# Performance work log

Hardware: AMD Instinct MI355X
Metric: run time of the kernel (lower is better)

The kernel has to match this reference:

```python
import jax, jax.numpy as jnp
from jax import lax
import numpy as np

B, N, NPOINTS, DOWN_NUM, K = 4, 4096, 4096, 1024, 16
EPS = 1e-5


def setup_inputs() -> dict:
    key = jax.random.key(0)
    ks = jax.random.split(key, 8)
    w = lambda k, s: jax.random.normal(k, s, jnp.float32) * 0.05
    return {
        "x": jax.random.normal(ks[0], (B, 3, N), jnp.float32),
        "w_in": w(ks[1], (8, 3)), "b_in": jnp.zeros((8,), jnp.float32),
        "w1": w(ks[2], (32, 16)), "g1w": jnp.ones((32,), jnp.float32), "g1b": jnp.zeros((32,), jnp.float32),
        "w2": w(ks[3], (64, 64)), "g2w": jnp.ones((64,), jnp.float32), "g2b": jnp.zeros((64,), jnp.float32),
        "w3": w(ks[4], (64, 128)), "g3w": jnp.ones((64,), jnp.float32), "g3b": jnp.zeros((64,), jnp.float32),
        "w4": w(ks[5], (128, 128)), "g4w": jnp.ones((128,), jnp.float32), "g4b": jnp.zeros((128,), jnp.float32),
    }


def _knn_idx(coor_k, coor_q, k):
    # coor_*: (B,3,N) -> idx (B,Nq,k) of k nearest points in coor_k for each query
    q = coor_q.transpose(0, 2, 1)  # (B,Nq,3)
    r = coor_k.transpose(0, 2, 1)  # (B,Nk,3)
    d = (jnp.sum(q * q, -1)[:, :, None] + jnp.sum(r * r, -1)[:, None, :]
         - 2.0 * jnp.einsum('bqc,bkc->bqk', q, r))
    _, idx = lax.top_k(-d, k)  # smallest distances
    return idx


def _graph_feature(coor_q, x_q, coor_k, x_k, k):
    # gather k-NN neighbor features and concat (neighbor - center, center)
    idx = _knn_idx(coor_k, coor_q, k)           # (B,Nq,k)
    xk = x_k.transpose(0, 2, 1)                  # (B,Nk,C)
    b, nq, _ = idx.shape
    c = xk.shape[-1]
    feat = jnp.take_along_axis(xk, idx.reshape(b, nq * k)[..., None], axis=1)
    feat = feat.reshape(b, nq, k, c).transpose(0, 3, 1, 2)  # (B,C,Nq,k)
    xq = x_q[:, :, :, None]                      # (B,C,Nq,1)
    return jnp.concatenate([feat - xq, jnp.broadcast_to(xq, feat.shape)], axis=1)


def _fps_idx(xyz, m):
    # furthest point sampling, xyz (B,N,3) -> idx (B,m); starts at point 0
    b, n, _ = xyz.shape
    def body(carry, _):
        dists, farthest = carry
        centroid = jnp.take_along_axis(xyz, farthest[:, None, None], axis=1)  # (B,1,3)
        d = jnp.sum((xyz - centroid) ** 2, axis=-1)
        dists = jnp.minimum(dists, d)
        return (dists, jnp.argmax(dists, axis=-1)), farthest
    init = (jnp.full((b, n), 1e10, xyz.dtype), jnp.zeros((b,), jnp.int32))
    _, idx = lax.scan(body, init, None, length=m)
    return idx.T  # (B,m)


def _fps_downsample(coor, f, m):
    idx = _fps_idx(coor.transpose(0, 2, 1), m)        # (B,m)
    combined = jnp.concatenate([coor, f], axis=1)      # (B,3+C,N)
    new = jnp.take_along_axis(combined, idx[:, None, :], axis=2)
    return new[:, :3], new[:, 3:]


def _group_norm(x, w, b, groups=4):
    bsz, c = x.shape[0], x.shape[1]
    xr = x.reshape(bsz, groups, -1)
    m = xr.mean(-1, keepdims=True)
    v = xr.var(-1, keepdims=True)
    xn = ((xr - m) * lax.rsqrt(v + EPS)).reshape(x.shape)
    shp = (1, c) + (1,) * (x.ndim - 2)
    return xn * w.reshape(shp) + b.reshape(shp)


def _block(f, w, gw, gb):
    # 1x1 conv (no bias) -> GroupNorm(4) -> LeakyReLU(0.2) -> max over neighbors
    h = jnp.einsum('oc,bcnk->bonk', w, f)
    h = jax.nn.leaky_relu(_group_norm(h, gw, gb), negative_slope=0.2)
    return h.max(axis=-1)


def reference(x, w_in, b_in, w1, g1w, g1b, w2, g2w, g2b, w3, g3w, g3b, w4, g4w, g4b):
    coor = x
    f = jnp.einsum('oc,bcn->bon', w_in, x) + b_in[None, :, None]
    inpc_f = f
    f = _graph_feature(coor, f, coor, f, K)
    f = _block(f, w1, g1w, g1b)                      # (B,32,N)
    coor_q, f_q = _fps_downsample(coor, f, NPOINTS // 2)
    f = _graph_feature(coor_q, f_q, coor, f, K)
    f = _block(f, w2, g2w, g2b)                      # (B,64,N/2)
    xyz1, point1 = coor_q, f
    coor = coor_q
    f = _graph_feature(coor, f, coor, f, K)
    f = _block(f, w3, g3w, g3b)                      # (B,64,N/2)
    coor_q, f_q = _fps_downsample(coor, f, DOWN_NUM)
    f = _graph_feature(coor_q, f_q, coor, f, K)
    f = _block(f, w4, g4w, g4b)                      # (B,128,DOWN_NUM)
    coor = coor_q
    return (coor, f, xyz1, point1, inpc_f)
```

## Files before the change

### kernel.cpp

```cpp
#include <hip/hip_runtime.h>
#include <float.h>
#include <math.h>

static constexpr int BATCH = 4;
static constexpr int NPT0  = 4096;

static constexpr size_t OFF_F0T  = 0;
static constexpr size_t OFF_F1T  = 524288;
static constexpr size_t OFF_F2T  = 3670016;
static constexpr size_t OFF_F3T  = 5767168;
static constexpr size_t OFF_CQ1  = 8912896;
static constexpr size_t OFF_CQ2  = 9011200;
static constexpr size_t OFF_H    = 9060352;
static constexpr size_t OFF_IDX1 = 42614784;
static constexpr size_t OFF_IDX2 = 43663360;
static constexpr size_t OFF_IDX3 = 44187648;
static constexpr size_t OFF_IDX4 = 44711936;
static constexpr size_t OFF_FPS1 = 44974080;
static constexpr size_t OFF_FPS2 = 45006848;
static constexpr size_t OFF_WD1  = 45023232;
static constexpr size_t OFF_WD2  = 45024256;
static constexpr size_t OFF_WD3  = 45032448;
static constexpr size_t OFF_WD4  = 45048832;
static constexpr size_t OFF_STAT = 45081600;
static constexpr size_t OFF_PART  = 45099008;
static constexpr size_t OFF_PART2 = OFF_PART;
static constexpr size_t OFF_PART3 = OFF_PART + 4194304;
static constexpr size_t OFF_PART4 = OFF_PART + 6291456;
static constexpr size_t OFF_CAND0 = 53487616;
static constexpr size_t OFF_CAND1 = 53749760;

static constexpr size_t OUT_COOR = 0;
static constexpr size_t OUT_F    = 12288;
static constexpr size_t OUT_XYZ1 = 536576;
static constexpr size_t OUT_PT1  = 561152;
static constexpr size_t OUT_INPC = 1085440;

template<int CTRL>
__device__ __forceinline__ unsigned long long dpp_max64(unsigned long long k) {
  unsigned lo = (unsigned)k, hi = (unsigned)(k >> 32);
  unsigned olo = (unsigned)__builtin_amdgcn_update_dpp((int)lo, (int)lo, CTRL, 0xF, 0xF, false);
  unsigned ohi = (unsigned)__builtin_amdgcn_update_dpp((int)hi, (int)hi, CTRL, 0xF, 0xF, false);
  unsigned long long o = ((unsigned long long)ohi << 32) | olo;
  return o > k ? o : k;
}

__device__ __forceinline__ void prep_dev(
    int vb, const float* __restrict__ w1, const float* __restrict__ w2,
    const float* __restrict__ w3, const float* __restrict__ w4,
    float* __restrict__ wd1, float* __restrict__ wd2,
    float* __restrict__ wd3, float* __restrict__ wd4,
    double* __restrict__ stats)
{
  int t = vb * 256 + threadIdx.x;
  if (t < 128) stats[t] = 0.0;
  if (t < 32 * 8)   { int o = t / 8,  c = t % 8;  wd1[t] = w1[o*16  + 8   + c] - w1[o*16  + c]; }
  if (t < 64 * 32)  { int o = t / 32, c = t % 32; wd2[t] = w2[o*64  + 32  + c] - w2[o*64  + c]; }
  if (t < 64 * 64)  { int o = t / 64, c = t % 64; wd3[t] = w3[o*128 + 64  + c] - w3[o*128 + c]; }
  if (t < 128 * 64) { int o = t / 64, c = t % 64; wd4[t] = w4[o*128 + 64  + c] - w4[o*128 + c]; }
}

__device__ __forceinline__ void linear_dev(
    int vb, const float* __restrict__ x, const float* __restrict__ w_in,
    const float* __restrict__ b_in, float* __restrict__ f0t,
    float* __restrict__ out_inpc)
{
  int t = vb * 256 + threadIdx.x;
  int n = t & (NPT0 - 1);
  int b = t >> 12;
  float x0 = x[(size_t)b*3*NPT0 + n];
  float x1 = x[(size_t)b*3*NPT0 + NPT0 + n];
  float x2 = x[(size_t)b*3*NPT0 + 2*NPT0 + n];
#pragma unroll
  for (int o = 0; o < 8; ++o) {
    float v = __fmul_rn(w_in[o*3], x0);
    v = fmaf(w_in[o*3+1], x1, v);
    v = fmaf(w_in[o*3+2], x2, v);
    v = __fadd_rn(v, b_in[o]);
    f0t[(size_t)t * 8 + o] = v;
    out_inpc[((size_t)b*8 + o)*NPT0 + n] = v;
  }
}

template<int CS>
__device__ __forceinline__ void knnp_pack_dev(
    int vb, const float* __restrict__ cq, const float4* __restrict__ candPack,
    unsigned long long* __restrict__ part, int Nq, int Nk)
{
  const int slices = Nk / CS;
  int s  = vb % slices;
  int r  = vb / slices;
  int qb = r % (Nq >> 8);
  int b  = r / (Nq >> 8);
  int t  = threadIdx.x;
  int q  = qb*256 + t;
  const float* cqb = cq + (size_t)b*3*Nq;
  float qx = cqb[q], qy = cqb[Nq + q], qz = cqb[2*Nq + q];
  float sqq = __fadd_rn(__fadd_rn(__fmul_rn(qx,qx), __fmul_rn(qy,qy)), __fmul_rn(qz,qz));

  const float4* cp = candPack + (size_t)b*Nk + s*CS;
  int jbase = s*CS;

  unsigned long long bd[16];
#pragma unroll
  for (int sl = 0; sl < 16; ++sl) bd[sl] = ~0ull;
  unsigned long long wk = ~0ull; int ws = 0;

#pragma unroll 4
  for (int jj = 0; jj < CS; ++jj) {
    float4 c = cp[jj];
    float dot = __fmul_rn(c.x, qx);
    dot = fmaf(c.y, qy, dot);
    dot = fmaf(c.z, qz, dot);
    float d = __fsub_rn(__fadd_rn(sqq, c.w), __fmul_rn(2.0f, dot));
    unsigned u = __float_as_uint(d);
    u ^= (0x80000000u | (unsigned)((int)u >> 31));
    unsigned long long key = ((unsigned long long)u << 32) | (unsigned)(jbase + jj);
    if (key < wk) {
      unsigned long long nw = 0; int nws = 0;
#pragma unroll
      for (int sl = 0; sl < 16; ++sl) {
        bool rep = (sl == ws);
        unsigned long long v = rep ? key : bd[sl];
        bd[sl] = v;
        bool g = v > nw;
        nw = g ? v : nw; nws = g ? sl : nws;
      }
      wk = nw; ws = nws;
    }
  }
  unsigned long long* op = part + (((size_t)b*Nq + q)*(size_t)slices + s)*16;
#pragma unroll
  for (int sl = 0; sl < 16; ++sl) op[sl] = bd[sl];
}

__device__ __forceinline__ void knnp_lds_dev(
    int vb, const float* __restrict__ cq, const float* __restrict__ ck,
    unsigned long long* __restrict__ part, int Nq, int Nk, int slices, void* smem)
{
  const int CS = 512;
  int s  = vb % slices;
  int r  = vb / slices;
  int qb = r % (Nq >> 8);
  int b  = r / (Nq >> 8);
  float4* cand = (float4*)smem;
  int t = threadIdx.x;
  const float* ckb = ck + (size_t)b*3*Nk;
  for (int jj = t; jj < CS; jj += 256) {
    int j = s*CS + jj;
    float xx = ckb[j], yy = ckb[Nk + j], zz = ckb[2*Nk + j];
    float sq = __fadd_rn(__fadd_rn(__fmul_rn(xx,xx), __fmul_rn(yy,yy)), __fmul_rn(zz,zz));
    cand[jj] = make_float4(xx, yy, zz, sq);
  }
  __syncthreads();
  int q = qb*256 + t;
  const float* cqb = cq + (size_t)b*3*Nq;
  float qx = cqb[q], qy = cqb[Nq + q], qz = cqb[2*Nq + q];
  float sqq = __fadd_rn(__fadd_rn(__fmul_rn(qx,qx), __fmul_rn(qy,qy)), __fmul_rn(qz,qz));

  unsigned long long bd[16];
#pragma unroll
  for (int sl = 0; sl < 16; ++sl) bd[sl] = ~0ull;
  unsigned long long wk = ~0ull; int ws = 0;

  for (int jj = 0; jj < CS; ++jj) {
    float4 c = cand[jj];
    float dot = __fmul_rn(c.x, qx);
    dot = fmaf(c.y, qy, dot);
    dot = fmaf(c.z, qz, dot);
    float d = __fsub_rn(__fadd_rn(sqq, c.w), __fmul_rn(2.0f, dot));
    unsigned u = __float_as_uint(d);
    u ^= (0x80000000u | (unsigned)((int)u >> 31));
    unsigned long long key = ((unsigned long long)u << 32) | (unsigned)(s*CS + jj);
    if (key < wk) {
      unsigned long long nw = 0; int nws = 0;
#pragma unroll
      for (int sl = 0; sl < 16; ++sl) {
        bool rep = (sl == ws);
        unsigned long long v = rep ? key : bd[sl];
        bd[sl] = v;
        bool g = v > nw;
        nw = g ? v : nw; nws = g ? sl : nws;
      }
      wk = nw; ws = nws;
    }
  }
  unsigned long long* op = part + (((size_t)b*Nq + q)*(size_t)slices + s)*16;
#pragma unroll
  for (int sl = 0; sl < 16; ++sl) op[sl] = bd[sl];
}

__device__ __forceinline__ void merge_dev(
    int vb, const unsigned long long* __restrict__ part, int* __restrict__ idx,
    int slices)
{
  int t = vb * 256 + threadIdx.x;
  const unsigned long long* ip = part + (size_t)t * slices * 16;
  unsigned long long bd[16];
#pragma unroll
  for (int sl = 0; sl < 16; ++sl) bd[sl] = ~0ull;
  unsigned long long wk = ~0ull; int ws = 0;
  int n = slices * 16;
  for (int i = 0; i < n; ++i) {
    unsigned long long key = ip[i];
    if (key < wk) {
      unsigned long long nw = 0; int nws = 0;
#pragma unroll
      for (int sl = 0; sl < 16; ++sl) {
        bool rep = (sl == ws);
        unsigned long long v = rep ? key : bd[sl];
        bd[sl] = v;
        bool g = v > nw;
        nw = g ? v : nw; nws = g ? sl : nws;
      }
      wk = nw; ws = nws;
    }
  }
  int* op = idx + (size_t)t * 16;
#pragma unroll
  for (int sl = 0; sl < 16; ++sl) op[sl] = (int)(bd[sl] & 0xFFFFFFFFull);
}

template<int NN, int PPT>
__device__ __forceinline__ void fps_dev(
    int b, const float* __restrict__ coor, int m, int* __restrict__ fidx_all,
    float* __restrict__ ca_all, float* __restrict__ co_all, void* smem)
{
  float* sx = (float*)smem;
  float* sy = sx + NN;
  float* sz = sy + NN;
  unsigned long long* part = (unsigned long long*)(sz + NN);
  int t = threadIdx.x, lane = t & 63, wv = t >> 6;
  const float* cb = coor + (size_t)b*3*NN;
  float px[PPT], py[PPT], pz[PPT], pd[PPT];
#pragma unroll
  for (int i = 0; i < PPT; ++i) {
    int j = i*256 + t;
    px[i] = cb[j]; py[i] = cb[NN + j]; pz[i] = cb[2*NN + j];
    pd[i] = 1e10f;
    sx[j] = px[i]; sy[j] = py[i]; sz[j] = pz[i];
  }
  __syncthreads();
  float cx = sx[0], cy = sy[0], cz = sz[0];
  int* fidx = fidx_all + b*m;
  float* ca = ca_all + (size_t)b*3*m;
  float* co = co_all + (size_t)b*3*m;
  int cur = 0, par = 0;
  for (int it = 0; it < m; ++it) {
    if (t == 0) {
      fidx[it] = cur;
      ca[it] = cx; ca[m + it] = cy; ca[2*m + it] = cz;
      co[it] = cx; co[m + it] = cy; co[2*m + it] = cz;
    }
    float bv = -1.0f; int bslot = 0;
#pragma unroll
    for (int i = 0; i < PPT; ++i) {
      float dx = __fsub_rn(px[i], cx);
      float dy = __fsub_rn(py[i], cy);
      float dz = __fsub_rn(pz[i], cz);
      float d = __fadd_rn(__fadd_rn(__fmul_rn(dx,dx), __fmul_rn(dy,dy)), __fmul_rn(dz,dz));
      float nd = fminf(pd[i], d);
      pd[i] = nd;
      bool g = nd > bv;
      bv = g ? nd : bv;
      bslot = g ? i : bslot;
    }
    unsigned bij = ~(unsigned)((bslot << 8) | t);
    unsigned long long k = ((unsigned long long)__float_as_uint(bv) << 32) | bij;
    k = dpp_max64<0x111>(k);
    k = dpp_max64<0x112>(k);
    k = dpp_max64<0x114>(k);
    k = dpp_max64<0x118>(k);
    k = dpp_max64<0x142>(k);
    k = dpp_max64<0x143>(k);
    unsigned wlo = (unsigned)__builtin_amdgcn_readlane((int)(unsigned)k, 63);
    unsigned whi = (unsigned)__builtin_amdgcn_readlane((int)(unsigned)(k >> 32), 63);
    if (lane == 0) part[par*4 + wv] = ((unsigned long long)whi << 32) | wlo;
    __syncthreads();
    unsigned long long k0 = part[par*4 + 0], k1 = part[par*4 + 1];
    unsigned long long k2 = part[par*4 + 2], k3 = part[par*4 + 3];
    k0 = k1 > k0 ? k1 : k0;
    k2 = k3 > k2 ? k3 : k2;
    k0 = k2 > k0 ? k2 : k0;
    cur = (int)(~(unsigned)(k0 & 0xFFFFFFFFull));
    cx = sx[cur]; cy = sy[cur]; cz = sz[cur];
    par ^= 1;
  }
}

template<int C, int COUT, int OC>
__device__ __forceinline__ void passA_dev(
    int vb, const float* __restrict__ xq, const float* __restrict__ xk,
    const int* __restrict__ idx, const float* __restrict__ w,
    const float* __restrict__ wdl, float* __restrict__ h,
    double* __restrict__ stats, int Nq, int Nk,
    const int* __restrict__ qmap, int NqSrc, void* smem)
{
  constexpr int NCH = COUT / OC;
  constexpr int GS  = COUT / 4;
  float* sxq   = (float*)smem;
  float* sbase = sxq + 16*C;
  int qb = Nq >> 4;
  int b = vb / qb, nb = vb % qb;
  int n0 = nb << 4;
  int t = threadIdx.x;
  for (int i = t; i < 16*C; i += 256) {
    int nn = i / C, cc = i % C;
    int qrow = qmap ? qmap[b*Nq + n0 + nn] : (n0 + nn);
    sxq[nn*C + cc] = xq[((size_t)b*NqSrc + qrow)*C + cc];
  }
  __syncthreads();
  for (int i = t; i < 16*COUT; i += 256) {
    int nn = i / COUT, o = i % COUT;
    float acc = 0.f;
#pragma unroll 4
    for (int c = 0; c < C; ++c) acc = fmaf(wdl[o*C + c], sxq[nn*C + c], acc);
    sbase[nn*(COUT+1) + o] = acc;
  }
  __syncthreads();
  int lane = t & 63;
  int n_loc = t >> 4, kk = t & 15;
  int kidx = idx[((size_t)b*Nq + n0 + n_loc)*16 + kk];
  const float* xr = xk + ((size_t)b*Nk + kidx)*C;
  float* hrow = h + (((size_t)b*Nq + n0 + n_loc)*16 + kk)*(size_t)COUT;
#pragma unroll 1
  for (int oc = 0; oc < NCH; ++oc) {
    int o0 = oc * OC;
    float acc[OC];
#pragma unroll
    for (int oi = 0; oi < OC; ++oi) acc[oi] = sbase[n_loc*(COUT+1) + o0 + oi];
#pragma unroll 1
    for (int c4 = 0; c4 < C/4; ++c4) {
      float4 v = *(const float4*)(xr + c4*4);
#pragma unroll
      for (int oi = 0; oi < OC; ++oi) {
        const float* wr = w + (size_t)(o0 + oi)*(2*C) + c4*4;
        acc[oi] = fmaf(wr[0], v.x, acc[oi]);
        acc[oi] = fmaf(wr[1], v.y, acc[oi]);
        acc[oi] = fmaf(wr[2], v.z, acc[oi]);
        acc[oi] = fmaf(wr[3], v.w, acc[oi]);
      }
    }
#pragma unroll
    for (int oi = 0; oi < OC; ++oi) hrow[o0 + oi] = acc[oi];
    double s = 0.0, s2 = 0.0;
#pragma unroll
    for (int oi = 0; oi < OC; ++oi) { double dv = (double)acc[oi]; s += dv; s2 += dv*dv; }
#pragma unroll
    for (int mm = 1; mm < 64; mm <<= 1) {
      s  += __shfl_xor(s,  mm, 64);
      s2 += __shfl_xor(s2, mm, 64);
    }
    if (lane == 0) {
      int g = o0 / GS;
      atomicAdd(&stats[((size_t)b*4 + g)*2],     s);
      atomicAdd(&stats[((size_t)b*4 + g)*2 + 1], s2);
    }
  }
}

template<int C, int COUT, int OC>
__global__ __launch_bounds__(256) void k_passA(
    const float* __restrict__ xq, const float* __restrict__ xk,
    const int* __restrict__ idx, const float* __restrict__ w,
    const float* __restrict__ wdl, float* __restrict__ h,
    double* __restrict__ stats, int Nq, int Nk,
    const int* __restrict__ qmap, int NqSrc)
{
  extern __shared__ char smem[];
  passA_dev<C,COUT,OC>(blockIdx.x, xq, xk, idx, w, wdl, h, stats, Nq, Nk,
                       qmap, NqSrc, smem);
}

__device__ __forceinline__ void passB_dev(
    int vb, const float* __restrict__ h, const double* __restrict__ stats,
    const float* __restrict__ gw, const float* __restrict__ gb,
    float* __restrict__ ft, float* __restrict__ ocn, int Nq, int COUT)
{
  int t = vb * 256 + threadIdx.x;
  int o = t % COUT;
  int r = t / COUT;
  int n = r % Nq;
  int b = r / Nq;
  int GS = COUT / 4, g = o / GS;
  double cnt = (double)GS * (double)Nq * 16.0;
  double su = stats[((size_t)b*4 + g)*2];
  double s2 = stats[((size_t)b*4 + g)*2 + 1];
  double mean = su / cnt;
  double var = s2 / cnt - mean * mean;
  float vf = (float)var; if (vf < 0.f) vf = 0.f;
  float inv = 1.0f / sqrtf(vf + 1e-5f);
  float A = gw[o] * inv;
  float Bb = gb[o] - (float)mean * A;
  const float* hp = h + (((size_t)b*Nq + n)*16)*(size_t)COUT + o;
  float m = -FLT_MAX;
#pragma unroll
  for (int k = 0; k < 16; ++k) {
    float v = hp[(size_t)k*COUT];
    float y = fmaf(v, A, Bb);
    y = (y >= 0.f) ? y : 0.2f*y;
    m = fmaxf(m, y);
  }
  if (ft)  ft[((size_t)b*Nq + n)*COUT + o] = m;
  if (ocn) ocn[((size_t)b*COUT + o)*Nq + n] = m;
}

__global__ __launch_bounds__(256) void k_passB(
    const float* __restrict__ h, const double* __restrict__ stats,
    const float* __restrict__ gw, const float* __restrict__ gb,
    float* __restrict__ ft, float* __restrict__ ocn, int Nq, int COUT)
{
  passB_dev(blockIdx.x, h, stats, gw, gb, ft, ocn, Nq, COUT);
}

__global__ __launch_bounds__(256) void k_pre(
    const float* __restrict__ x, const float* __restrict__ w_in,
    const float* __restrict__ b_in, float* __restrict__ f0t,
    float* __restrict__ outInpc,
    const float* __restrict__ w1, const float* __restrict__ w2,
    const float* __restrict__ w3, const float* __restrict__ w4,
    float* __restrict__ wd1, float* __restrict__ wd2,
    float* __restrict__ wd3, float* __restrict__ wd4,
    double* __restrict__ stats, float4* __restrict__ cand0)
{
  int vb = blockIdx.x;
  if (vb < 64) {
    int g = vb*256 + threadIdx.x;
    int b = g >> 12, n = g & 4095;
    const float* xb = x + (size_t)b*3*4096;
    float xx = xb[n], yy = xb[4096 + n], zz = xb[2*4096 + n];
    float sq = __fadd_rn(__fadd_rn(__fmul_rn(xx,xx), __fmul_rn(yy,yy)), __fmul_rn(zz,zz));
    cand0[g] = make_float4(xx, yy, zz, sq);
  }
  else if (vb < 96) prep_dev(vb - 64, w1, w2, w3, w4, wd1, wd2, wd3, wd4, stats);
  else              linear_dev(vb - 96, x, w_in, b_in, f0t, outInpc);
}

__global__ __launch_bounds__(256, 2) void k_megaA(
    const float* __restrict__ x, int* __restrict__ fps1,
    float* __restrict__ cq1, float* __restrict__ outXyz1,
    const float4* __restrict__ cand0, unsigned long long* __restrict__ part1)
{
  extern __shared__ char smem[];
  int vb = blockIdx.x;
  if (vb < 4) fps_dev<4096,16>(vb, x, 2048, fps1, cq1, outXyz1, smem);
  else        knnp_pack_dev<1024>(vb - 4, x, cand0, part1, 4096, 4096);
}

__global__ __launch_bounds__(256) void k_mergeP(
    const unsigned long long* __restrict__ part1, int* __restrict__ idx1,
    const float* __restrict__ cq1, float4* __restrict__ cand1)
{
  int vb = blockIdx.x;
  if (vb < 64) merge_dev(vb, part1, idx1, 4);
  else {
    int g = (vb - 64)*256 + threadIdx.x;
    int b = g >> 11, n = g & 2047;
    const float* cb = cq1 + (size_t)b*3*2048;
    float xx = cb[n], yy = cb[2048 + n], zz = cb[2*2048 + n];
    float sq = __fadd_rn(__fadd_rn(__fmul_rn(xx,xx), __fmul_rn(yy,yy)), __fmul_rn(zz,zz));
    cand1[g] = make_float4(xx, yy, zz, sq);
  }
}

__global__ __launch_bounds__(256, 2) void k_megaB(
    const float* __restrict__ cq1, const float4* __restrict__ cand0,
    const float4* __restrict__ cand1,
    int* __restrict__ fps2, float* __restrict__ cq2, float* __restrict__ outCoor,
    unsigned long long* __restrict__ part2, unsigned long long* __restrict__ part3,
    const float* __restrict__ f0t, const int* __restrict__ idx1,
    const float* __restrict__ w1, const float* __restrict__ wd1,
    float* __restrict__ h, double* __restrict__ st1)
{
  extern __shared__ char smem[];
  int vb = blockIdx.x;
  if      (vb < 4)          fps_dev<2048,8>(vb, cq1, 1024, fps2, cq2, outCoor, smem);
  else if (vb < 4 + 128)    knnp_pack_dev<1024>(vb - 4,   cq1, cand0, part2, 2048, 4096);
  else if (vb < 4 + 128+64) knnp_pack_dev<1024>(vb - 132, cq1, cand1, part3, 2048, 2048);
  else                      passA_dev<8,32,8>(vb - 196, f0t, f0t, idx1, w1, wd1,
                                              h, st1, 4096, 4096, nullptr, 4096, smem);
}

__global__ __launch_bounds__(256) void k_megaC(
    const float* __restrict__ cq2, const float* __restrict__ cq1,
    unsigned long long* __restrict__ part4,
    const unsigned long long* __restrict__ part2, int* __restrict__ idx2,
    const unsigned long long* __restrict__ part3, int* __restrict__ idx3,
    const float* __restrict__ h, const double* __restrict__ st1,
    const float* __restrict__ g1w, const float* __restrict__ g1b,
    float* __restrict__ f1t)
{
  extern __shared__ char smem[];
  int vb = blockIdx.x;
  if      (vb < 64)  knnp_lds_dev(vb, cq2, cq1, part4, 1024, 2048, 4, smem);
  else if (vb < 96)  merge_dev(vb - 64, part2, idx2, 4);
  else if (vb < 128) merge_dev(vb - 96, part3, idx3, 2);
  else               passB_dev(vb - 128, h, st1, g1w, g1b, f1t, nullptr, 4096, 32);
}

__global__ __launch_bounds__(256) void k_megaD(
    const unsigned long long* __restrict__ part4, int* __restrict__ idx4,
    const float* __restrict__ f1t, const int* __restrict__ idx2,
    const float* __restrict__ w2, const float* __restrict__ wd2,
    float* __restrict__ h, double* __restrict__ st2,
    const int* __restrict__ fps1)
{
  extern __shared__ char smem[];
  int vb = blockIdx.x;
  if (vb < 16) merge_dev(vb, part4, idx4, 4);
  else         passA_dev<32,64,16>(vb - 16, f1t, f1t, idx2, w2, wd2, h, st2,
                                   2048, 4096, fps1, 4096, smem);
}

extern "C" void kernel_launch(void* const* d_in, const int* in_sizes, int n_in,
                              void* d_out, int out_size, void* d_ws, size_t ws_size,
                              hipStream_t stream)
{
  (void)in_sizes; (void)n_in; (void)out_size; (void)ws_size;
  const float* x    = (const float*)d_in[0];
  const float* w_in = (const float*)d_in[1];
  const float* b_in = (const float*)d_in[2];
  const float* w1   = (const float*)d_in[3];
  const float* g1w  = (const float*)d_in[4];
  const float* g1b  = (const float*)d_in[5];
  const float* w2   = (const float*)d_in[6];
  const float* g2w  = (const float*)d_in[7];
  const float* g2b  = (const float*)d_in[8];
  const float* w3   = (const float*)d_in[9];
  const float* g3w  = (const float*)d_in[10];
  const float* g3b  = (const float*)d_in[11];
  const float* w4   = (const float*)d_in[12];
  const float* g4w  = (const float*)d_in[13];
  const float* g4b  = (const float*)d_in[14];
  float* out = (float*)d_out;
  char*  wsb = (char*)d_ws;

  float* f0t  = (float*)(wsb + OFF_F0T);
  float* f1t  = (float*)(wsb + OFF_F1T);
  float* f2t  = (float*)(wsb + OFF_F2T);
  float* f3t  = (float*)(wsb + OFF_F3T);
  float* cq1  = (float*)(wsb + OFF_CQ1);
  float* cq2  = (float*)(wsb + OFF_CQ2);
  float* h    = (float*)(wsb + OFF_H);
  int*   idx1 = (int*)(wsb + OFF_IDX1);
  int*   idx2 = (int*)(wsb + OFF_IDX2);
  int*   idx3 = (int*)(wsb + OFF_IDX3);
  int*   idx4 = (int*)(wsb + OFF_IDX4);
  int*   fps1 = (int*)(wsb + OFF_FPS1);
  int*   fps2 = (int*)(wsb + OFF_FPS2);
  float* wd1  = (float*)(wsb + OFF_WD1);
  float* wd2  = (float*)(wsb + OFF_WD2);
  float* wd3  = (float*)(wsb + OFF_WD3);
  float* wd4  = (float*)(wsb + OFF_WD4);
  double* statAll = (double*)(wsb + OFF_STAT);
  double* st1 = statAll, *st2 = statAll + 32, *st3 = statAll + 64, *st4 = statAll + 96;
  unsigned long long* part1 = (unsigned long long*)(wsb + OFF_PART);
  unsigned long long* part2 = (unsigned long long*)(wsb + OFF_PART2);
  unsigned long long* part3 = (unsigned long long*)(wsb + OFF_PART3);
  unsigned long long* part4 = (unsigned long long*)(wsb + OFF_PART4);
  float4* cand0 = (float4*)(wsb + OFF_CAND0);
  float4* cand1 = (float4*)(wsb + OFF_CAND1);

  float* outCoor = out + OUT_COOR;
  float* outF    = out + OUT_F;
  float* outXyz1 = out + OUT_XYZ1;
  float* outPt1  = out + OUT_PT1;
  float* outInpc = out + OUT_INPC;

  k_pre<<<160, 256, 0, stream>>>(x, w_in, b_in, f0t, outInpc,
      w1, w2, w3, w4, wd1, wd2, wd3, wd4, statAll, cand0);

  k_megaA<<<260, 256, 49216, stream>>>(x, fps1, cq1, outXyz1, cand0, part1);

  k_mergeP<<<96, 256, 0, stream>>>(part1, idx1, cq1, cand1);

  k_megaB<<<1220, 256, 24640, stream>>>(
      cq1, cand0, cand1, fps2, cq2, outCoor, part2, part3, f0t, idx1, w1, wd1, h, st1);

  k_megaC<<<2176, 256, 8192, stream>>>(
      cq2, cq1, part4, part2, idx2, part3, idx3, h, st1, g1w, g1b, f1t);

  k_megaD<<<528, 256, 6208, stream>>>(part4, idx4, f1t, idx2, w2, wd2, h, st2, fps1);

  k_passB<<<2048, 256, 0, stream>>>(h, st2, g2w, g2b, f2t, outPt1, 2048, 64);
  k_passA<64,64,16><<<512, 256, 8256, stream>>>(f2t, f2t, idx3, w3, wd3, h, st3,
                                                2048, 2048, nullptr, 2048);
  k_passB<<<2048, 256, 0, stream>>>(h, st3, g3w, g3b, f3t, nullptr, 2048, 64);
  k_passA<64,128,16><<<256, 256, 12352, stream>>>(f3t, f3t, idx4, w4, wd4, h, st4,
                                                  1024, 2048, fps2, 2048);
  k_passB<<<2048, 256, 0, stream>>>(h, st4, g4w, g4b, nullptr, outF, 1024, 128);
}
```

Baseline: 3.037 ms.

## Widen FPS and KNN mega-kernel blocks to 512 threads

Furthest point sampling now runs with 512 threads per block instead of 256. Each thread holds half as many points, and the cross-wave argmax reduction loops over 8 wave partials. The KNN partial kernels handle 512 queries per block, and two 256-thread passA sub-blocks are packed into one 512-thread block, each with its own shared-memory region. The goal is to shorten the serial FPS iteration chain and reduce the number of blocks launched. The cost is a wider per-iteration reduction, the loss of the 2-blocks-per-CU occupancy hint, and a dependence on any unshown code in the KNN path that may still assume 256 threads.

```diff
diff --git a/kernel.cpp b/kernel.cpp
--- a/kernel.cpp
+++ b/kernel.cpp
@@ -83,17 +83,17 @@
 }
 
 template<int CS>
-__device__ __forceinline__ void knnp_pack_dev(
+__device__ __forceinline__ void knnp_pack_dev512(
     int vb, const float* __restrict__ cq, const float4* __restrict__ candPack,
     unsigned long long* __restrict__ part, int Nq, int Nk)
 {
   const int slices = Nk / CS;
   int s  = vb % slices;
   int r  = vb / slices;
-  int qb = r % (Nq >> 8);
-  int b  = r / (Nq >> 8);
+  int qb = r % (Nq >> 9);
+  int b  = r / (Nq >> 9);
   int t  = threadIdx.x;
-  int q  = qb*256 + t;
+  int q  = qb*512 + t;
   const float* cqb = cq + (size_t)b*3*Nq;
   float qx = cqb[q], qy = cqb[Nq + q], qz = cqb[2*Nq + q];
   float sqq = __fadd_rn(__fadd_rn(__fmul_rn(qx,qx), __fmul_rn(qy,qy)), __fmul_rn(qz,qz));
@@ -221,11 +221,12 @@
   for (int sl = 0; sl < 16; ++sl) op[sl] = (int)(bd[sl] & 0xFFFFFFFFull);
 }
 
-template<int NN, int PPT>
+template<int NN, int PPT, int NTHR>
 __device__ __forceinline__ void fps_dev(
     int b, const float* __restrict__ coor, int m, int* __restrict__ fidx_all,
     float* __restrict__ ca_all, float* __restrict__ co_all, void* smem)
 {
+  constexpr int WAVES = NTHR / 64;
   float* sx = (float*)smem;
   float* sy = sx + NN;
   float* sz = sy + NN;
@@ -235,7 +236,7 @@
   float px[PPT], py[PPT], pz[PPT], pd[PPT];
 #pragma unroll
   for (int i = 0; i < PPT; ++i) {
-    int j = i*256 + t;
+    int j = i*NTHR + t;
     px[i] = cb[j]; py[i] = cb[NN + j]; pz[i] = cb[2*NN + j];
     pd[i] = 1e10f;
     sx[j] = px[i]; sy[j] = py[i]; sz[j] = pz[i];
@@ -265,7 +266,7 @@
       bv = g ? nd : bv;
       bslot = g ? i : bslot;
     }
-    unsigned bij = ~(unsigned)((bslot << 8) | t);
+    unsigned bij = ~(unsigned)(bslot * NTHR + t);
     unsigned long long k = ((unsigned long long)__float_as_uint(bv) << 32) | bij;
     k = dpp_max64<0x111>(k);
     k = dpp_max64<0x112>(k);
@@ -275,13 +276,14 @@
     k = dpp_max64<0x143>(k);
     unsigned wlo = (unsigned)__builtin_amdgcn_readlane((int)(unsigned)k, 63);
     unsigned whi = (unsigned)__builtin_amdgcn_readlane((int)(unsigned)(k >> 32), 63);
-    if (lane == 0) part[par*4 + wv] = ((unsigned long long)whi << 32) | wlo;
+    if (lane == 0) part[par*WAVES + wv] = ((unsigned long long)whi << 32) | wlo;
     __syncthreads();
-    unsigned long long k0 = part[par*4 + 0], k1 = part[par*4 + 1];
-    unsigned long long k2 = part[par*4 + 2], k3 = part[par*4 + 3];
-    k0 = k1 > k0 ? k1 : k0;
-    k2 = k3 > k2 ? k3 : k2;
-    k0 = k2 > k0 ? k2 : k0;
+    unsigned long long k0 = part[par*WAVES + 0];
+#pragma unroll
+    for (int w = 1; w < WAVES; ++w) {
+      unsigned long long kw = part[par*WAVES + w];
+      k0 = kw > k0 ? kw : k0;
+    }
     cur = (int)(~(unsigned)(k0 & 0xFFFFFFFFull));
     cx = sx[cur]; cy = sy[cur]; cz = sz[cur];
     par ^= 1;
@@ -290,7 +292,7 @@
 
 template<int C, int COUT, int OC>
 __device__ __forceinline__ void passA_dev(
-    int vb, const float* __restrict__ xq, const float* __restrict__ xk,
+    int vb, int tid, const float* __restrict__ xq, const float* __restrict__ xk,
     const int* __restrict__ idx, const float* __restrict__ w,
     const float* __restrict__ wdl, float* __restrict__ h,
     double* __restrict__ stats, int Nq, int Nk,
@@ -303,7 +305,7 @@
   int qb = Nq >> 4;
   int b = vb / qb, nb = vb % qb;
   int n0 = nb << 4;
-  int t = threadIdx.x;
+  int t = tid;
   for (int i = t; i < 16*C; i += 256) {
     int nn = i / C, cc = i % C;
     int qrow = qmap ? qmap[b*Nq + n0 + nn] : (n0 + nn);
@@ -368,8 +370,8 @@
     const int* __restrict__ qmap, int NqSrc)
 {
   extern __shared__ char smem[];
-  passA_dev<C,COUT,OC>(blockIdx.x, xq, xk, idx, w, wdl, h, stats, Nq, Nk,
-                       qmap, NqSrc, smem);
+  passA_dev<C,COUT,OC>(blockIdx.x, threadIdx.x, xq, xk, idx, w, wdl, h, stats,
+                       Nq, Nk, qmap, NqSrc, smem);
 }
 
 __device__ __forceinline__ void passB_dev(
@@ -436,15 +438,15 @@
   else              linear_dev(vb - 96, x, w_in, b_in, f0t, outInpc);
 }
 
-__global__ __launch_bounds__(256, 2) void k_megaA(
+__global__ __launch_bounds__(512) void k_megaA(
     const float* __restrict__ x, int* __restrict__ fps1,
     float* __restrict__ cq1, float* __restrict__ outXyz1,
     const float4* __restrict__ cand0, unsigned long long* __restrict__ part1)
 {
   extern __shared__ char smem[];
   int vb = blockIdx.x;
-  if (vb < 4) fps_dev<4096,16>(vb, x, 2048, fps1, cq1, outXyz1, smem);
-  else        knnp_pack_dev<1024>(vb - 4, x, cand0, part1, 4096, 4096);
+  if (vb < 4) fps_dev<4096,8,512>(vb, x, 2048, fps1, cq1, outXyz1, smem);
+  else        knnp_pack_dev512<1024>(vb - 4, x, cand0, part1, 4096, 4096);
 }
 
 __global__ __launch_bounds__(256) void k_mergeP(
@@ -463,7 +465,7 @@
   }
 }
 
-__global__ __launch_bounds__(256, 2) void k_megaB(
+__global__ __launch_bounds__(512) void k_megaB(
     const float* __restrict__ cq1, const float4* __restrict__ cand0,
     const float4* __restrict__ cand1,
     int* __restrict__ fps2, float* __restrict__ cq2, float* __restrict__ outCoor,
@@ -474,11 +476,16 @@
 {
   extern __shared__ char smem[];
   int vb = blockIdx.x;
-  if      (vb < 4)          fps_dev<2048,8>(vb, cq1, 1024, fps2, cq2, outCoor, smem);
-  else if (vb < 4 + 128)    knnp_pack_dev<1024>(vb - 4,   cq1, cand0, part2, 2048, 4096);
-  else if (vb < 4 + 128+64) knnp_pack_dev<1024>(vb - 132, cq1, cand1, part3, 2048, 2048);
-  else                      passA_dev<8,32,8>(vb - 196, f0t, f0t, idx1, w1, wd1,
-                                              h, st1, 4096, 4096, nullptr, 4096, smem);
+  if      (vb < 4)         fps_dev<2048,4,512>(vb, cq1, 1024, fps2, cq2, outCoor, smem);
+  else if (vb < 4 + 64)    knnp_pack_dev512<1024>(vb - 4,  cq1, cand0, part2, 2048, 4096);
+  else if (vb < 4 + 64+32) knnp_pack_dev512<1024>(vb - 68, cq1, cand1, part3, 2048, 2048);
+  else {
+    int sub = threadIdx.x >> 8;
+    int tid = threadIdx.x & 255;
+    int vpa = (vb - 100)*2 + sub;
+    passA_dev<8,32,8>(vpa, tid, f0t, f0t, idx1, w1, wd1,
+                      h, st1, 4096, 4096, nullptr, 4096, smem + sub*2624);
+  }
 }
 
 __global__ __launch_bounds__(256) void k_megaC(
@@ -508,8 +515,8 @@
   extern __shared__ char smem[];
   int vb = blockIdx.x;
   if (vb < 16) merge_dev(vb, part4, idx4, 4);
-  else         passA_dev<32,64,16>(vb - 16, f1t, f1t, idx2, w2, wd2, h, st2,
-                                   2048, 4096, fps1, 4096, smem);
+  else         passA_dev<32,64,16>(vb - 16, threadIdx.x, f1t, f1t, idx2, w2, wd2,
+                                   h, st2, 2048, 4096, fps1, 4096, smem);
 }
 
 extern "C" void kernel_launch(void* const* d_in, const int* in_sizes, int n_in,
@@ -570,11 +577,11 @@
   k_pre<<<160, 256, 0, stream>>>(x, w_in, b_in, f0t, outInpc,
       w1, w2, w3, w4, wd1, wd2, wd3, wd4, statAll, cand0);
 
-  k_megaA<<<260, 256, 49216, stream>>>(x, fps1, cq1, outXyz1, cand0, part1);
+  k_megaA<<<132, 512, 49280, stream>>>(x, fps1, cq1, outXyz1, cand0, part1);
 
   k_mergeP<<<96, 256, 0, stream>>>(part1, idx1, cq1, cand1);
 
-  k_megaB<<<1220, 256, 24640, stream>>>(
+  k_megaB<<<612, 512, 24704, stream>>>(
       cq1, cand0, cand1, fps2, cq2, outCoor, part2, part3, f0t, idx1, w1, wd1, h, st1);
 
   k_megaC<<<2176, 256, 8192, stream>>>(
```

Result: slower. 3.692 ms (+21.6%).
